# Kernel tuning notes

Measured on AMD Instinct MI355X. Metric: run time of the kernel, lower is better.

## Reference

```python
import jax, jax.numpy as jnp
import numpy as np

N = 100000
E = 3200000
T = 8
F = 64


def _temporal_conv(x, src, dst, time_index, W, b):
    # time-bucketed segmented scatter-add: segment id = dst*T + t
    seg = dst * T + time_index                      # [E]
    msgs = x[src]                                   # [E, F] gather (x_j)
    agg = jax.ops.segment_sum(msgs, seg, num_segments=N * T)  # [N*T, F]
    cat = agg.reshape(N, T * x.shape[-1])           # concat over t blocks: [N, T*F]
    return jax.nn.relu(cat @ W + b)                 # temporal_lin + relu


def setup_inputs() -> dict:
    key = jax.random.key(0)
    ks = jax.random.split(key, 10)
    x = jax.random.normal(ks[0], (N, F), dtype=jnp.float32)
    edge_index = jax.random.randint(ks[1], (2, E), 0, N, dtype=jnp.int64)
    time_index = jax.random.randint(ks[2], (E,), 0, T, dtype=jnp.int64)
    s1 = 1.0 / np.sqrt(F * T)
    W1 = jax.random.uniform(ks[3], (F * T, 64), jnp.float32, -s1, s1)
    b1 = jax.random.uniform(ks[4], (64,), jnp.float32, -s1, s1)
    s2 = 1.0 / np.sqrt(64 * T)
    W2 = jax.random.uniform(ks[5], (64 * T, 64), jnp.float32, -s2, s2)
    b2 = jax.random.uniform(ks[6], (64,), jnp.float32, -s2, s2)
    s3 = 1.0 / np.sqrt(64)
    Wssl = jax.random.uniform(ks[7], (64, F), jnp.float32, -s3, s3)
    bssl = jax.random.uniform(ks[8], (F,), jnp.float32, -s3, s3)
    return {"x": x, "edge_index": edge_index, "time_index": time_index,
            "W1": W1, "b1": b1, "W2": W2, "b2": b2, "Wssl": Wssl, "bssl": bssl}


def reference(x, edge_index, time_index, W1, b1, W2, b2, Wssl, bssl):
    src, dst = edge_index[0], edge_index[1]  # flow source_to_target
    h = _temporal_conv(x, src, dst, time_index, W1, b1)
    h = jax.nn.relu(h)                        # outer relu in TemporalSSTGNN.forward
    h = _temporal_conv(h, src, dst, time_index, W2, b2)
    ssl = h @ Wssl + bssl                     # self_supervised_linear
    return (h, ssl)
```

## Files before the change

### kernel.cpp

```cpp
#include <hip/hip_runtime.h>
#include <hip/hip_bf16.h>

#define N_NODES 100000
#define N_EDGES 3200000
#define NB 391
#define NBP 400
#define CAP 9216
#define PCAP 20480
#define ZNODE N_NODES
#define NTILES 6250
#define AROW 520

typedef __attribute__((ext_vector_type(8))) short short8;
typedef __attribute__((ext_vector_type(4))) float floatx4;

__device__ __forceinline__ float bf2f(unsigned short u) {
    unsigned int x = ((unsigned int)u) << 16;
    return __builtin_bit_cast(float, x);
}
__device__ __forceinline__ unsigned short f2bf(float f) {
    unsigned int u = __builtin_bit_cast(unsigned int, f);
    unsigned int r = (u + 0x7FFFu + ((u >> 16) & 1u)) >> 16;
    return (unsigned short)r;
}


__global__ __launch_bounds__(512) void k_init(int* __restrict__ cursor) {
    int tid = threadIdx.x;
    if (tid < NB) cursor[tid] = tid * CAP;
}

__global__ __launch_bounds__(1024) void k_bscatter(const int* __restrict__ ei,
                                                   const int* __restrict__ ti,
                                                   int* __restrict__ cursor,
                                                   unsigned int* __restrict__ words) {
    __shared__ int h[NBP];
    __shared__ int bb[NBP];
    int tid = threadIdx.x;
    if (tid < NBP) h[tid] = 0;
    __syncthreads();
    int base = blockIdx.x * 4096;
    int breg[4], ofs[4];
    unsigned wreg[4];
#pragma unroll
    for (int i = 0; i < 4; ++i) {
        int e = base + i * 1024 + tid;
        bool v = e < N_EDGES;
        int dst = v ? ei[N_EDGES + e] : 0;
        int src = v ? ei[e] : 0;
        int tt  = v ? ti[e] : 0;
        int b = dst >> 8;
        breg[i] = v ? b : -1;
        wreg[i] = ((unsigned)src << 11) | ((unsigned)(dst & 255) << 3) | (unsigned)tt;
        ofs[i] = v ? atomicAdd(&h[b], 1) : 0;
    }
    __syncthreads();
    if (tid < NB) {
        int c = h[tid];
        bb[tid] = c ? atomicAdd(&cursor[tid], c) : 0;
    }
    __syncthreads();
#pragma unroll
    for (int i = 0; i < 4; ++i)
        if (breg[i] >= 0) words[bb[breg[i]] + ofs[i]] = wreg[i];
}

__global__ __launch_bounds__(1024) void k_lsort(const int* __restrict__ cursor,
                                                const unsigned int* __restrict__ words,
                                                int2* __restrict__ node_pm,
                                                int* __restrict__ gid_pad) {
    __shared__ int h[2048];
    __shared__ int ps[1024];
    __shared__ int nb[256];
    int tid = threadIdx.x;
    int b = blockIdx.x;
    int rb = b * CAP, re = cursor[b];
    h[tid] = 0; h[tid + 1024] = 0;
    __syncthreads();
    unsigned wreg[9];
    int ofs[9];
#pragma unroll
    for (int i = 0; i < 9; ++i) {
        int e = rb + i * 1024 + tid;
        bool v = e < re;
        unsigned w = v ? words[e] : 0u;
        wreg[i] = w;
        ofs[i] = v ? atomicAdd(&h[w & 2047u], 1) : -1;
    }
    __syncthreads();
    int sz = 0;
    if (tid < 256) {
        int m = 0;
#pragma unroll
        for (int t = 0; t < 8; ++t) { int c = h[tid * 8 + t]; m = c > m ? c : m; }
        m = (m + 1) & ~1;
        sz = m * 8;
    }
    ps[tid] = sz;
    __syncthreads();
    for (int off = 1; off < 1024; off <<= 1) {
        int t = (tid >= off) ? ps[tid - off] : 0;
        __syncthreads();
        ps[tid] += t;
        __syncthreads();
    }
    if (tid < 256) nb[tid] = ps[tid] - sz;
    __syncthreads();
    int bsz = ps[1023];
    int pbase = b * PCAP;
    for (int s = tid; s < bsz; s += 1024) gid_pad[pbase + s] = ZNODE;
    int gn = b * 256 + tid;
    if (tid < 256 && gn < N_NODES) node_pm[gn] = (int2){pbase + nb[tid], sz >> 3};
    __syncthreads();
#pragma unroll
    for (int i = 0; i < 9; ++i)
        if (ofs[i] >= 0) {
            unsigned w = wreg[i];
            int ls = (int)(w & 2047u);
            gid_pad[pbase + nb[ls >> 3] + ofs[i] * 8 + (ls & 7)] = (int)(w >> 11);
        }
}


__global__ void k_cvt(const float* __restrict__ x, unsigned short* __restrict__ xb,
                      unsigned short* __restrict__ h1b) {
    int i = blockIdx.x * 256 + threadIdx.x;
    if (i < N_NODES * 64) xb[i] = f2bf(x[i]);
    if (i < 64) {
        xb[(size_t)ZNODE * 64 + i] = 0;
        h1b[(size_t)ZNODE * 64 + i] = 0;
    }
}

__global__ void k_wprep(const float* __restrict__ W1, const float* __restrict__ W2,
                        const float* __restrict__ Wssl,
                        unsigned short* __restrict__ Wf1, unsigned short* __restrict__ Wf2,
                        unsigned short* __restrict__ Wsf) {
    int i = blockIdx.x * 256 + threadIdx.x;
    if (i < 512 * 64) {
        int k = i >> 6, o = i & 63;
        int c = o >> 4, m = o & 15;
        int ks = k >> 5, q = (k >> 3) & 3, j = k & 7;
        int pos = (((c * 16 + ks) * 64) + (m + 16 * q)) * 8 + j;
        Wf1[pos] = f2bf(W1[i]);
        Wf2[pos] = f2bf(W2[i]);
    }
    if (i < 64 * 64) {
        int k = i >> 6, o = i & 63;
        int c = o >> 4, m = o & 15;
        int ks = k >> 5, q = (k >> 3) & 3, j = k & 7;
        int pos = (((c * 2 + ks) * 64) + (m + 16 * q)) * 8 + j;
        Wsf[pos] = f2bf(Wssl[i]);
    }
}


__global__ __launch_bounds__(512) void k_fused(const int2* __restrict__ node_pm,
                                               const int* __restrict__ gid_pad,
                                               const unsigned short* __restrict__ xb,
                                               const unsigned short* __restrict__ Wf,
                                               const float* __restrict__ bias,
                                               unsigned short* __restrict__ out_bf,
                                               float* __restrict__ out_f32) {
    __shared__ __align__(16) unsigned short Atile[32 * AROW];
    int tid = threadIdx.x;
    int wave = tid >> 6, lane = tid & 63;
    int node_base = blockIdx.x * 32;
    int tl = lane >> 3, fo = lane & 7;
    const uint4* xs = (const uint4*)xb;

    for (int i = 0; i < 4; ++i) {
        int nl = wave * 4 + i;
        int n = node_base + nl;
        int2 pm = node_pm[n];
        int pb = __builtin_amdgcn_readfirstlane(pm.x);
        int ml = __builtin_amdgcn_readfirstlane(pm.y);
        const int* gp = gid_pad + pb + tl;
        float acc[8] = {0.f, 0.f, 0.f, 0.f, 0.f, 0.f, 0.f, 0.f};
        for (int k = 0; k < ml; k += 2) {
            int g0 = gp[k * 8];
            int g1 = gp[k * 8 + 8];
            uint4 p0 = xs[((unsigned)g0 << 3) + fo];
            uint4 p1 = xs[((unsigned)g1 << 3) + fo];
            acc[0] += __builtin_bit_cast(float, p0.x << 16);
            acc[1] += __builtin_bit_cast(float, p0.x & 0xFFFF0000u);
            acc[2] += __builtin_bit_cast(float, p0.y << 16);
            acc[3] += __builtin_bit_cast(float, p0.y & 0xFFFF0000u);
            acc[4] += __builtin_bit_cast(float, p0.z << 16);
            acc[5] += __builtin_bit_cast(float, p0.z & 0xFFFF0000u);
            acc[6] += __builtin_bit_cast(float, p0.w << 16);
            acc[7] += __builtin_bit_cast(float, p0.w & 0xFFFF0000u);
            acc[0] += __builtin_bit_cast(float, p1.x << 16);
            acc[1] += __builtin_bit_cast(float, p1.x & 0xFFFF0000u);
            acc[2] += __builtin_bit_cast(float, p1.y << 16);
            acc[3] += __builtin_bit_cast(float, p1.y & 0xFFFF0000u);
            acc[4] += __builtin_bit_cast(float, p1.z << 16);
            acc[5] += __builtin_bit_cast(float, p1.z & 0xFFFF0000u);
            acc[6] += __builtin_bit_cast(float, p1.w << 16);
            acc[7] += __builtin_bit_cast(float, p1.w & 0xFFFF0000u);
        }
        unsigned r0, r1, r2, r3;
        asm("v_cvt_pk_bf16_f32 %0, %1, %2" : "=v"(r0) : "v"(acc[0]), "v"(acc[1]));
        asm("v_cvt_pk_bf16_f32 %0, %1, %2" : "=v"(r1) : "v"(acc[2]), "v"(acc[3]));
        asm("v_cvt_pk_bf16_f32 %0, %1, %2" : "=v"(r2) : "v"(acc[4]), "v"(acc[5]));
        asm("v_cvt_pk_bf16_f32 %0, %1, %2" : "=v"(r3) : "v"(acc[6]), "v"(acc[7]));
        uint4 st;
        st.x = r0; st.y = r1; st.z = r2; st.w = r3;
        *(uint4*)(&Atile[nl * AROW + tl * 64 + fo * 8]) = st;
    }
    __syncthreads();

    int nt = wave >> 2, c = wave & 3;
    int m = lane & 15, q = lane >> 4;
    floatx4 acc = (floatx4){0.f, 0.f, 0.f, 0.f};
    const short8* wf8 = (const short8*)Wf;
    const unsigned short* abase = &Atile[(nt * 16 + m) * AROW + q * 8];
#pragma unroll
    for (int ks = 0; ks < 16; ++ks) {
        short8 a = *(const short8*)(abase + ks * 32);
        short8 b = wf8[(c * 16 + ks) * 64 + lane];
        acc = __builtin_amdgcn_mfma_f32_16x16x32_bf16(a, b, acc, 0, 0, 0);
    }
    float bb = bias[c * 16 + m];
    int node0 = node_base + nt * 16;
#pragma unroll
    for (int i = 0; i < 4; ++i) {
        float v = acc[i] + bb;
        v = v > 0.f ? v : 0.f;
        int node = node0 + q * 4 + i;
        size_t idx = (size_t)node * 64 + c * 16 + m;
        if (out_bf)  out_bf[idx] = f2bf(v);
        if (out_f32) out_f32[idx] = v;
    }
}


__global__ __launch_bounds__(256) void k_sslm(const unsigned short* __restrict__ h2b,
                                              const unsigned short* __restrict__ Wsf,
                                              const float* __restrict__ bssl,
                                              float* __restrict__ out) {
    int wave = threadIdx.x >> 6, lane = threadIdx.x & 63;
    int tile = blockIdx.x * 4 + wave;
    if (tile >= NTILES) return;
    int m = lane & 15, q = lane >> 4;
    const unsigned short* arow = h2b + ((size_t)(tile * 16 + m)) * 64 + q * 8;
    floatx4 acc[4];
    for (int c = 0; c < 4; ++c) acc[c] = (floatx4){0.f, 0.f, 0.f, 0.f};
    const short8* wf8 = (const short8*)Wsf;
#pragma unroll
    for (int ks = 0; ks < 2; ++ks) {
        short8 a = *(const short8*)(arow + ks * 32);
#pragma unroll
        for (int c = 0; c < 4; ++c) {
            short8 b = wf8[(c * 2 + ks) * 64 + lane];
            acc[c] = __builtin_amdgcn_mfma_f32_16x16x32_bf16(a, b, acc[c], 0, 0, 0);
        }
    }
    int node0 = tile * 16;
#pragma unroll
    for (int c = 0; c < 4; ++c) {
        float bb = bssl[c * 16 + m];
#pragma unroll
        for (int i = 0; i < 4; ++i) {
            int node = node0 + q * 4 + i;
            out[(size_t)node * 64 + c * 16 + m] = acc[c][i] + bb;
        }
    }
}


extern "C" void kernel_launch(void* const* d_in, const int* in_sizes, int n_in,
                              void* d_out, int out_size, void* d_ws, size_t ws_size,
                              hipStream_t stream) {
    const float* x    = (const float*)d_in[0];
    const int*   ei   = (const int*)d_in[1];
    const int*   ti   = (const int*)d_in[2];
    const float* W1   = (const float*)d_in[3];
    const float* b1   = (const float*)d_in[4];
    const float* W2   = (const float*)d_in[5];
    const float* b2   = (const float*)d_in[6];
    const float* Wssl = (const float*)d_in[7];
    const float* bssl = (const float*)d_in[8];
    float* out = (float*)d_out;

    char* w = (char*)d_ws;
    auto alloc = [&](size_t bytes) -> char* {
        char* p = w;
        w += (bytes + 255) & ~(size_t)255;
        return p;
    };
    int* cursor   = (int*)alloc((size_t)NBP * 4);
    unsigned int* words = (unsigned int*)alloc((size_t)NB * CAP * 4);
    int2* node_pm = (int2*)alloc((size_t)N_NODES * 8);
    int* gid_pad  = (int*)alloc((size_t)NB * PCAP * 4);
    unsigned short* xb  = (unsigned short*)alloc((size_t)(N_NODES + 1) * 64 * 2);
    unsigned short* h1b = (unsigned short*)alloc((size_t)(N_NODES + 1) * 64 * 2);
    unsigned short* h2b = (unsigned short*)alloc((size_t)N_NODES * 64 * 2);
    unsigned short* Wf1 = (unsigned short*)alloc((size_t)512 * 64 * 2);
    unsigned short* Wf2 = (unsigned short*)alloc((size_t)512 * 64 * 2);
    unsigned short* Wsf = (unsigned short*)alloc((size_t)64 * 64 * 2);

    k_init<<<1, 512, 0, stream>>>(cursor);
    k_bscatter<<<(N_EDGES + 4095) / 4096, 1024, 0, stream>>>(ei, ti, cursor, words);
    k_lsort<<<NB, 1024, 0, stream>>>(cursor, words, node_pm, gid_pad);
    k_cvt<<<(N_NODES * 64 + 255) / 256, 256, 0, stream>>>(x, xb, h1b);
    k_wprep<<<(512 * 64 + 255) / 256, 256, 0, stream>>>(W1, W2, Wssl, Wf1, Wf2, Wsf);

    k_fused<<<N_NODES / 32, 512, 0, stream>>>(node_pm, gid_pad, xb, Wf1, b1, h1b, nullptr);
    k_fused<<<N_NODES / 32, 512, 0, stream>>>(node_pm, gid_pad, h1b, Wf2, b2, h2b, out);

    k_sslm<<<(NTILES + 3) / 4, 256, 0, stream>>>(h2b, Wsf, bssl, out + (size_t)N_NODES * 64);
}
```

Before: 339.9 us.

## Transpose padded neighbor layout per time slot and vectorize gather index loads

The padded neighbor index layout changes from interleaved-by-time to a contiguous run per time slot, padded to multiples of 4 with a minimum of 8. The aggregation loop can then load four indices at once with int4 reads and keep eight row gathers in flight per iteration. The node metadata loads are also hoisted out of the per-node loop. Separately, the cursor init kernel is replaced by a memset and the weight-prep kernel is merged into the conversion kernel to cut launches. The cost is extra padding: more dummy gathers of the zero row, and a larger padded footprint that could approach the per-bucket capacity.

```diff
diff --git a/kernel.cpp b/kernel.cpp
--- a/kernel.cpp
+++ b/kernel.cpp
@@ -24,11 +24,6 @@
     return (unsigned short)r;
 }
 
-
-__global__ __launch_bounds__(512) void k_init(int* __restrict__ cursor) {
-    int tid = threadIdx.x;
-    if (tid < NB) cursor[tid] = tid * CAP;
-}
 
 __global__ __launch_bounds__(1024) void k_bscatter(const int* __restrict__ ei,
                                                    const int* __restrict__ ti,
@@ -62,7 +57,10 @@
     __syncthreads();
 #pragma unroll
     for (int i = 0; i < 4; ++i)
-        if (breg[i] >= 0) words[bb[breg[i]] + ofs[i]] = wreg[i];
+        if (breg[i] >= 0) {
+            int b = breg[i];
+            words[b * CAP + bb[b] + ofs[i]] = wreg[i];
+        }
 }
 
 __global__ __launch_bounds__(1024) void k_lsort(const int* __restrict__ cursor,
@@ -72,9 +70,10 @@
     __shared__ int h[2048];
     __shared__ int ps[1024];
     __shared__ int nb[256];
+    __shared__ int s_ml[256];
     int tid = threadIdx.x;
     int b = blockIdx.x;
-    int rb = b * CAP, re = cursor[b];
+    int rb = b * CAP, re = rb + cursor[b];
     h[tid] = 0; h[tid + 1024] = 0;
     __syncthreads();
     unsigned wreg[9];
@@ -93,7 +92,9 @@
         int m = 0;
 #pragma unroll
         for (int t = 0; t < 8; ++t) { int c = h[tid * 8 + t]; m = c > m ? c : m; }
-        m = (m + 1) & ~1;
+        m = (m + 3) & ~3;
+        if (m < 8) m = 8;
+        s_ml[tid] = m;
         sz = m * 8;
     }
     ps[tid] = sz;
@@ -110,33 +111,31 @@
     int pbase = b * PCAP;
     for (int s = tid; s < bsz; s += 1024) gid_pad[pbase + s] = ZNODE;
     int gn = b * 256 + tid;
-    if (tid < 256 && gn < N_NODES) node_pm[gn] = (int2){pbase + nb[tid], sz >> 3};
+    if (tid < 256 && gn < N_NODES) node_pm[gn] = (int2){pbase + nb[tid], s_ml[tid]};
     __syncthreads();
 #pragma unroll
     for (int i = 0; i < 9; ++i)
         if (ofs[i] >= 0) {
             unsigned w = wreg[i];
             int ls = (int)(w & 2047u);
-            gid_pad[pbase + nb[ls >> 3] + ofs[i] * 8 + (ls & 7)] = (int)(w >> 11);
+            int nd = ls >> 3, t = ls & 7;
+            gid_pad[pbase + nb[nd] + t * s_ml[nd] + ofs[i]] = (int)(w >> 11);
         }
 }
 
 
 __global__ void k_cvt(const float* __restrict__ x, unsigned short* __restrict__ xb,
-                      unsigned short* __restrict__ h1b) {
+                      unsigned short* __restrict__ h1b,
+                      const float* __restrict__ W1, const float* __restrict__ W2,
+                      const float* __restrict__ Wssl,
+                      unsigned short* __restrict__ Wf1, unsigned short* __restrict__ Wf2,
+                      unsigned short* __restrict__ Wsf) {
     int i = blockIdx.x * 256 + threadIdx.x;
     if (i < N_NODES * 64) xb[i] = f2bf(x[i]);
     if (i < 64) {
         xb[(size_t)ZNODE * 64 + i] = 0;
         h1b[(size_t)ZNODE * 64 + i] = 0;
     }
-}
-
-__global__ void k_wprep(const float* __restrict__ W1, const float* __restrict__ W2,
-                        const float* __restrict__ Wssl,
-                        unsigned short* __restrict__ Wf1, unsigned short* __restrict__ Wf2,
-                        unsigned short* __restrict__ Wsf) {
-    int i = blockIdx.x * 256 + threadIdx.x;
     if (i < 512 * 64) {
         int k = i >> 6, o = i & 63;
         int c = o >> 4, m = o & 15;
@@ -154,6 +153,17 @@
     }
 }
 
+
+__device__ __forceinline__ void accum8(float* a, uint4 p) {
+    a[0] += __builtin_bit_cast(float, p.x << 16);
+    a[1] += __builtin_bit_cast(float, p.x & 0xFFFF0000u);
+    a[2] += __builtin_bit_cast(float, p.y << 16);
+    a[3] += __builtin_bit_cast(float, p.y & 0xFFFF0000u);
+    a[4] += __builtin_bit_cast(float, p.z << 16);
+    a[5] += __builtin_bit_cast(float, p.z & 0xFFFF0000u);
+    a[6] += __builtin_bit_cast(float, p.w << 16);
+    a[7] += __builtin_bit_cast(float, p.w & 0xFFFF0000u);
+}
 
 __global__ __launch_bounds__(512) void k_fused(const int2* __restrict__ node_pm,
                                                const int* __restrict__ gid_pad,
@@ -169,35 +179,40 @@
     int tl = lane >> 3, fo = lane & 7;
     const uint4* xs = (const uint4*)xb;
 
+    int2 pm[4];
+#pragma unroll
+    for (int i = 0; i < 4; ++i) pm[i] = node_pm[node_base + wave * 4 + i];
+
+#pragma unroll
     for (int i = 0; i < 4; ++i) {
         int nl = wave * 4 + i;
-        int n = node_base + nl;
-        int2 pm = node_pm[n];
-        int pb = __builtin_amdgcn_readfirstlane(pm.x);
-        int ml = __builtin_amdgcn_readfirstlane(pm.y);
-        const int* gp = gid_pad + pb + tl;
+        int pb = __builtin_amdgcn_readfirstlane(pm[i].x);
+        int ml = __builtin_amdgcn_readfirstlane(pm[i].y);
+        const int* gp = gid_pad + pb + tl * ml;
         float acc[8] = {0.f, 0.f, 0.f, 0.f, 0.f, 0.f, 0.f, 0.f};
-        for (int k = 0; k < ml; k += 2) {
-            int g0 = gp[k * 8];
-            int g1 = gp[k * 8 + 8];
-            uint4 p0 = xs[((unsigned)g0 << 3) + fo];
-            uint4 p1 = xs[((unsigned)g1 << 3) + fo];
-            acc[0] += __builtin_bit_cast(float, p0.x << 16);
-            acc[1] += __builtin_bit_cast(float, p0.x & 0xFFFF0000u);
-            acc[2] += __builtin_bit_cast(float, p0.y << 16);
-            acc[3] += __builtin_bit_cast(float, p0.y & 0xFFFF0000u);
-            acc[4] += __builtin_bit_cast(float, p0.z << 16);
-            acc[5] += __builtin_bit_cast(float, p0.z & 0xFFFF0000u);
-            acc[6] += __builtin_bit_cast(float, p0.w << 16);
-            acc[7] += __builtin_bit_cast(float, p0.w & 0xFFFF0000u);
-            acc[0] += __builtin_bit_cast(float, p1.x << 16);
-            acc[1] += __builtin_bit_cast(float, p1.x & 0xFFFF0000u);
-            acc[2] += __builtin_bit_cast(float, p1.y << 16);
-            acc[3] += __builtin_bit_cast(float, p1.y & 0xFFFF0000u);
-            acc[4] += __builtin_bit_cast(float, p1.z << 16);
-            acc[5] += __builtin_bit_cast(float, p1.z & 0xFFFF0000u);
-            acc[6] += __builtin_bit_cast(float, p1.w << 16);
-            acc[7] += __builtin_bit_cast(float, p1.w & 0xFFFF0000u);
+        int k = 0;
+#pragma unroll 1
+        for (; k + 8 <= ml; k += 8) {
+            int4 ga = *(const int4*)(gp + k);
+            int4 gb = *(const int4*)(gp + k + 4);
+            uint4 p0 = xs[((unsigned)ga.x << 3) + fo];
+            uint4 p1 = xs[((unsigned)ga.y << 3) + fo];
+            uint4 p2 = xs[((unsigned)ga.z << 3) + fo];
+            uint4 p3 = xs[((unsigned)ga.w << 3) + fo];
+            uint4 p4 = xs[((unsigned)gb.x << 3) + fo];
+            uint4 p5 = xs[((unsigned)gb.y << 3) + fo];
+            uint4 p6 = xs[((unsigned)gb.z << 3) + fo];
+            uint4 p7 = xs[((unsigned)gb.w << 3) + fo];
+            accum8(acc, p0); accum8(acc, p1); accum8(acc, p2); accum8(acc, p3);
+            accum8(acc, p4); accum8(acc, p5); accum8(acc, p6); accum8(acc, p7);
+        }
+        if (k < ml) {
+            int4 ga = *(const int4*)(gp + k);
+            uint4 p0 = xs[((unsigned)ga.x << 3) + fo];
+            uint4 p1 = xs[((unsigned)ga.y << 3) + fo];
+            uint4 p2 = xs[((unsigned)ga.z << 3) + fo];
+            uint4 p3 = xs[((unsigned)ga.w << 3) + fo];
+            accum8(acc, p0); accum8(acc, p1); accum8(acc, p2); accum8(acc, p3);
         }
         unsigned r0, r1, r2, r3;
         asm("v_cvt_pk_bf16_f32 %0, %1, %2" : "=v"(r0) : "v"(acc[0]), "v"(acc[1]));
@@ -300,11 +315,11 @@
     unsigned short* Wf2 = (unsigned short*)alloc((size_t)512 * 64 * 2);
     unsigned short* Wsf = (unsigned short*)alloc((size_t)64 * 64 * 2);
 
-    k_init<<<1, 512, 0, stream>>>(cursor);
+    hipMemsetAsync(cursor, 0, (size_t)NBP * 4, stream);
     k_bscatter<<<(N_EDGES + 4095) / 4096, 1024, 0, stream>>>(ei, ti, cursor, words);
     k_lsort<<<NB, 1024, 0, stream>>>(cursor, words, node_pm, gid_pad);
-    k_cvt<<<(N_NODES * 64 + 255) / 256, 256, 0, stream>>>(x, xb, h1b);
-    k_wprep<<<(512 * 64 + 255) / 256, 256, 0, stream>>>(W1, W2, Wssl, Wf1, Wf2, Wsf);
+    k_cvt<<<(N_NODES * 64 + 255) / 256, 256, 0, stream>>>(x, xb, h1b, W1, W2, Wssl,
+                                                          Wf1, Wf2, Wsf);
 
     k_fused<<<N_NODES / 32, 512, 0, stream>>>(node_pm, gid_pad, xb, Wf1, b1, h1b, nullptr);
     k_fused<<<N_NODES / 32, 512, 0, stream>>>(node_pm, gid_pad, h1b, Wf2, b2, h2b, out);
```

After: 323.7 us. -4.8%, faster.
